# Kernel optimization log

Hardware: AMD Instinct MI355X
Metric: run time of the kernel (lower is better)

## Reference

```python
import jax, jax.numpy as jnp
import numpy as np

B, C, H, W = 4, 48, 512, 512

def gaussian_kernel(kernel_size, channels):
    # matches torch get_gaussian_kernel: sigma from OpenCV rule
    sigma = 0.3 * ((kernel_size - 1) * 0.5 - 1) + 0.8
    grid = np.arange(kernel_size, dtype=np.float32) - kernel_size // 2
    k1 = np.exp(-grid ** 2 / (2 * sigma ** 2))
    k1 /= k1.sum()
    k2 = np.outer(k1, k1)  # [k,k]
    # OIHW depthwise: [C, 1, k, k]
    return jnp.asarray(np.broadcast_to(k2, (channels, 1, kernel_size, kernel_size)))

def depthwise_conv(x, kernel, pad):
    # x: [B,C,H,W], kernel: [C,1,k,k]
    return jax.lax.conv_general_dilated(
        x, kernel,
        window_strides=(1, 1),
        padding=((pad, pad), (pad, pad)),
        dimension_numbers=('NCHW', 'OIHW', 'NCHW'),
        feature_group_count=x.shape[1])

def setup_inputs() -> dict:
    key = jax.random.key(0)
    s = jax.random.normal(key, (B, C, H, W), dtype=jnp.float32)
    one = jnp.ones((), dtype=jnp.float32)
    return {'s': s, 'w1': one, 'w2': one, 'w3': one, 'w4': one}

def reference(s, w1, w2, w3, w4):
    channels = s.shape[1]
    k3 = gaussian_kernel(3, channels)
    k5 = gaussian_kernel(5, channels)
    k7 = gaussian_kernel(7, channels)
    s3 = depthwise_conv(s, k3, 1)
    s5 = depthwise_conv(s, k5, 2)
    s7 = depthwise_conv(s, k7, 3)
    # fused diff + weighted sum: w1*s + w2*(s-s3) + w3*(s3-s5) + w4*(s5-s7)
    return w1 * s + w2 * (s - s3) + w3 * (s3 - s5) + w4 * (s5 - s7)
```

## Files before the change

### kernel.cpp

```cpp
#include <hip/hip_runtime.h>
#include <math.h>

#define TX 64
#define TY 16
#define IN_W 72
#define IN_H 22

struct GaussCoefs {
    float g3[3];
    float g5[5];
    float g7[7];
};

__global__ __launch_bounds__(256) void mgdf_kernel(
    const float* __restrict__ s,
    const float* __restrict__ w1p, const float* __restrict__ w2p,
    const float* __restrict__ w3p, const float* __restrict__ w4p,
    float* __restrict__ out,
    GaussCoefs gc, int Wd, int Hd)
{
    __shared__ float in_tile[IN_H][IN_W];
    __shared__ float h3s[IN_H][TX];
    __shared__ float h5s[IN_H][TX];
    __shared__ float h7s[IN_H][TX];

    const int tid = threadIdx.x;
    const int plane = blockIdx.z;
    const int x0 = blockIdx.x * TX;
    const int y0 = blockIdx.y * TY;
    const float* sp = s + (size_t)plane * Hd * Wd;

    const float w1 = *w1p, w2 = *w2p, w3 = *w3p, w4 = *w4p;
    const float a0 = w1 + w2;
    const float a3 = w3 - w2;
    const float a5 = w4 - w3;
    const float a7 = -w4;

    for (int c = tid; c < (IN_W / 4) * IN_H; c += 256) {
        const int r  = c / (IN_W / 4);
        const int c4 = c % (IN_W / 4);
        const int gy = y0 - 3 + r;
        const int gx = x0 - 4 + c4 * 4;
        float4 v = make_float4(0.f, 0.f, 0.f, 0.f);
        if (gy >= 0 && gy < Hd) {
            const float* rowp = sp + (size_t)gy * Wd;
            if (gx >= 0 && gx + 3 < Wd) {
                v = *(const float4*)(rowp + gx);
            } else {
                float tmp[4];
                #pragma unroll
                for (int j = 0; j < 4; ++j) {
                    const int x = gx + j;
                    tmp[j] = (x >= 0 && x < Wd) ? rowp[x] : 0.f;
                }
                v = make_float4(tmp[0], tmp[1], tmp[2], tmp[3]);
            }
        }
        *(float4*)&in_tile[r][c4 * 4] = v;
    }
    __syncthreads();

    for (int task = tid; task < IN_H * (TX / 4); task += 256) {
        const int r  = task / (TX / 4);
        const int ch = task % (TX / 4);
        const float* row = &in_tile[r][ch * 4];
        const float4 va = *(const float4*)(row);
        const float4 vb = *(const float4*)(row + 4);
        const float4 vc = *(const float4*)(row + 8);
        const float v[12] = {va.x, va.y, va.z, va.w,
                             vb.x, vb.y, vb.z, vb.w,
                             vc.x, vc.y, vc.z, vc.w};
        float o3[4], o5[4], o7[4];
        #pragma unroll
        for (int j = 0; j < 4; ++j) {
            float h7 = 0.f;
            #pragma unroll
            for (int i = 0; i < 7; ++i) h7 = fmaf(gc.g7[i], v[j + 1 + i], h7);
            float h5 = 0.f;
            #pragma unroll
            for (int i = 0; i < 5; ++i) h5 = fmaf(gc.g5[i], v[j + 2 + i], h5);
            float h3 = 0.f;
            #pragma unroll
            for (int i = 0; i < 3; ++i) h3 = fmaf(gc.g3[i], v[j + 3 + i], h3);
            o3[j] = h3; o5[j] = h5; o7[j] = h7;
        }
        *(float4*)&h3s[r][ch * 4] = make_float4(o3[0], o3[1], o3[2], o3[3]);
        *(float4*)&h5s[r][ch * 4] = make_float4(o5[0], o5[1], o5[2], o5[3]);
        *(float4*)&h7s[r][ch * 4] = make_float4(o7[0], o7[1], o7[2], o7[3]);
    }
    __syncthreads();

    const int tx = tid & 15;
    const int ty = tid >> 4;
    const int xb = tx * 4;

    float acc3[4] = {0.f, 0.f, 0.f, 0.f};
    float acc5[4] = {0.f, 0.f, 0.f, 0.f};
    float acc7[4] = {0.f, 0.f, 0.f, 0.f};

    #pragma unroll
    for (int i = 0; i < 7; ++i) {
        const float4 hv = *(const float4*)&h7s[ty + i][xb];
        acc7[0] = fmaf(gc.g7[i], hv.x, acc7[0]);
        acc7[1] = fmaf(gc.g7[i], hv.y, acc7[1]);
        acc7[2] = fmaf(gc.g7[i], hv.z, acc7[2]);
        acc7[3] = fmaf(gc.g7[i], hv.w, acc7[3]);
    }
    #pragma unroll
    for (int i = 0; i < 5; ++i) {
        const float4 hv = *(const float4*)&h5s[ty + 1 + i][xb];
        acc5[0] = fmaf(gc.g5[i], hv.x, acc5[0]);
        acc5[1] = fmaf(gc.g5[i], hv.y, acc5[1]);
        acc5[2] = fmaf(gc.g5[i], hv.z, acc5[2]);
        acc5[3] = fmaf(gc.g5[i], hv.w, acc5[3]);
    }
    #pragma unroll
    for (int i = 0; i < 3; ++i) {
        const float4 hv = *(const float4*)&h3s[ty + 2 + i][xb];
        acc3[0] = fmaf(gc.g3[i], hv.x, acc3[0]);
        acc3[1] = fmaf(gc.g3[i], hv.y, acc3[1]);
        acc3[2] = fmaf(gc.g3[i], hv.z, acc3[2]);
        acc3[3] = fmaf(gc.g3[i], hv.w, acc3[3]);
    }

    const float4 sv = *(const float4*)&in_tile[ty + 3][xb + 4];
    float4 o;
    o.x = a0 * sv.x + a3 * acc3[0] + a5 * acc5[0] + a7 * acc7[0];
    o.y = a0 * sv.y + a3 * acc3[1] + a5 * acc5[1] + a7 * acc7[1];
    o.z = a0 * sv.z + a3 * acc3[2] + a5 * acc5[2] + a7 * acc7[2];
    o.w = a0 * sv.w + a3 * acc3[3] + a5 * acc5[3] + a7 * acc7[3];

    float* outp = out + (size_t)plane * Hd * Wd + (size_t)(y0 + ty) * Wd + x0 + xb;
    *(float4*)outp = o;
}

static void fill_gauss(float* g, int k) {
    const double sigma = 0.3 * ((k - 1) * 0.5 - 1.0) + 0.8;
    double t[7], sum = 0.0;
    for (int i = 0; i < k; ++i) {
        const double x = (double)(i - k / 2);
        t[i] = exp(-x * x / (2.0 * sigma * sigma));
        sum += t[i];
    }
    for (int i = 0; i < k; ++i) g[i] = (float)(t[i] / sum);
}

extern "C" void kernel_launch(void* const* d_in, const int* in_sizes, int n_in,
                              void* d_out, int out_size, void* d_ws, size_t ws_size,
                              hipStream_t stream) {
    const float* s  = (const float*)d_in[0];
    const float* w1 = (const float*)d_in[1];
    const float* w2 = (const float*)d_in[2];
    const float* w3 = (const float*)d_in[3];
    const float* w4 = (const float*)d_in[4];
    float* out = (float*)d_out;

    const int Hd = 512, Wd = 512;
    const int planes = in_sizes[0] / (Hd * Wd);

    GaussCoefs gc;
    fill_gauss(gc.g3, 3);
    fill_gauss(gc.g5, 5);
    fill_gauss(gc.g7, 7);

    dim3 grid(Wd / TX, Hd / TY, planes);
    mgdf_kernel<<<grid, 256, 0, stream>>>(s, w1, w2, w3, w4, out, gc, Wd, Hd);
}
```

Baseline: 372.9 us.

## Register-block vertical pass per thread and drop intermediate shared buffers

Each thread now computes eight output rows. It does the horizontal filter on the fly for each of 14 input rows and scatters the results into register accumulators, so the h3/h5/h7 shared arrays and the second barrier are gone. The block tile grows to 128 rows, which cuts the halo overhead from 22/16 to 134/128. The blend weights are folded into the vertical coefficients. In exchange register pressure rises (32 accumulators plus temporaries), the grid has fewer blocks, and the launch-bounds hint now asks for 4 blocks per CU.

```diff
diff --git a/kernel.cpp b/kernel.cpp
--- a/kernel.cpp
+++ b/kernel.cpp
@@ -1,10 +1,11 @@
 #include <hip/hip_runtime.h>
 #include <math.h>
 
-#define TX 64
-#define TY 16
+#define TX   64
+#define RPT  8
+#define TYB  (16 * RPT)
 #define IN_W 72
-#define IN_H 22
+#define IN_H (TYB + 6)
 
 struct GaussCoefs {
     float g3[3];
@@ -12,7 +13,7 @@
     float g7[7];
 };
 
-__global__ __launch_bounds__(256) void mgdf_kernel(
+__global__ __launch_bounds__(256, 4) void mgdf_kernel(
     const float* __restrict__ s,
     const float* __restrict__ w1p, const float* __restrict__ w2p,
     const float* __restrict__ w3p, const float* __restrict__ w4p,
@@ -20,14 +21,11 @@
     GaussCoefs gc, int Wd, int Hd)
 {
     __shared__ float in_tile[IN_H][IN_W];
-    __shared__ float h3s[IN_H][TX];
-    __shared__ float h5s[IN_H][TX];
-    __shared__ float h7s[IN_H][TX];
 
-    const int tid = threadIdx.x;
+    const int tid   = threadIdx.x;
     const int plane = blockIdx.z;
-    const int x0 = blockIdx.x * TX;
-    const int y0 = blockIdx.y * TY;
+    const int x0    = blockIdx.x * TX;
+    const int y0    = blockIdx.y * TYB;
     const float* sp = s + (size_t)plane * Hd * Wd;
 
     const float w1 = *w1p, w2 = *w2p, w3 = *w3p, w4 = *w4p;
@@ -36,7 +34,15 @@
     const float a5 = w4 - w3;
     const float a7 = -w4;
 
-    for (int c = tid; c < (IN_W / 4) * IN_H; c += 256) {
+    float w7v[7], w5v[5], w3v[3];
+    #pragma unroll
+    for (int i = 0; i < 7; ++i) w7v[i] = a7 * gc.g7[i];
+    #pragma unroll
+    for (int i = 0; i < 5; ++i) w5v[i] = a5 * gc.g5[i];
+    #pragma unroll
+    for (int i = 0; i < 3; ++i) w3v[i] = a3 * gc.g3[i];
+
+    for (int c = tid; c < IN_H * (IN_W / 4); c += 256) {
         const int r  = c / (IN_W / 4);
         const int c4 = c % (IN_W / 4);
         const int gy = y0 - 3 + r;
@@ -60,17 +66,28 @@
     }
     __syncthreads();
 
-    for (int task = tid; task < IN_H * (TX / 4); task += 256) {
-        const int r  = task / (TX / 4);
-        const int ch = task % (TX / 4);
-        const float* row = &in_tile[r][ch * 4];
+    const int tx  = tid & 15;
+    const int tyg = tid >> 4;
+    const int ty0 = tyg * RPT;
+    const int xb  = tx * 4;
+
+    float acc[RPT][4];
+    #pragma unroll
+    for (int r = 0; r < RPT; ++r) {
+        acc[r][0] = 0.f; acc[r][1] = 0.f; acc[r][2] = 0.f; acc[r][3] = 0.f;
+    }
+
+    #pragma unroll
+    for (int ri = 0; ri < RPT + 6; ++ri) {
+        const float* row = &in_tile[ty0 + ri][xb];
         const float4 va = *(const float4*)(row);
         const float4 vb = *(const float4*)(row + 4);
         const float4 vc = *(const float4*)(row + 8);
         const float v[12] = {va.x, va.y, va.z, va.w,
                              vb.x, vb.y, vb.z, vb.w,
                              vc.x, vc.y, vc.z, vc.w};
-        float o3[4], o5[4], o7[4];
+
+        float h3v[4], h5v[4], h7v[4], sv[4];
         #pragma unroll
         for (int j = 0; j < 4; ++j) {
             float h7 = 0.f;
@@ -82,56 +99,36 @@
             float h3 = 0.f;
             #pragma unroll
             for (int i = 0; i < 3; ++i) h3 = fmaf(gc.g3[i], v[j + 3 + i], h3);
-            o3[j] = h3; o5[j] = h5; o7[j] = h7;
+            h7v[j] = h7; h5v[j] = h5; h3v[j] = h3; sv[j] = v[j + 4];
         }
-        *(float4*)&h3s[r][ch * 4] = make_float4(o3[0], o3[1], o3[2], o3[3]);
-        *(float4*)&h5s[r][ch * 4] = make_float4(o5[0], o5[1], o5[2], o5[3]);
-        *(float4*)&h7s[r][ch * 4] = make_float4(o7[0], o7[1], o7[2], o7[3]);
-    }
-    __syncthreads();
 
-    const int tx = tid & 15;
-    const int ty = tid >> 4;
-    const int xb = tx * 4;
-
-    float acc3[4] = {0.f, 0.f, 0.f, 0.f};
-    float acc5[4] = {0.f, 0.f, 0.f, 0.f};
-    float acc7[4] = {0.f, 0.f, 0.f, 0.f};
-
-    #pragma unroll
-    for (int i = 0; i < 7; ++i) {
-        const float4 hv = *(const float4*)&h7s[ty + i][xb];
-        acc7[0] = fmaf(gc.g7[i], hv.x, acc7[0]);
-        acc7[1] = fmaf(gc.g7[i], hv.y, acc7[1]);
-        acc7[2] = fmaf(gc.g7[i], hv.z, acc7[2]);
-        acc7[3] = fmaf(gc.g7[i], hv.w, acc7[3]);
-    }
-    #pragma unroll
-    for (int i = 0; i < 5; ++i) {
-        const float4 hv = *(const float4*)&h5s[ty + 1 + i][xb];
-        acc5[0] = fmaf(gc.g5[i], hv.x, acc5[0]);
-        acc5[1] = fmaf(gc.g5[i], hv.y, acc5[1]);
-        acc5[2] = fmaf(gc.g5[i], hv.z, acc5[2]);
-        acc5[3] = fmaf(gc.g5[i], hv.w, acc5[3]);
-    }
-    #pragma unroll
-    for (int i = 0; i < 3; ++i) {
-        const float4 hv = *(const float4*)&h3s[ty + 2 + i][xb];
-        acc3[0] = fmaf(gc.g3[i], hv.x, acc3[0]);
-        acc3[1] = fmaf(gc.g3[i], hv.y, acc3[1]);
-        acc3[2] = fmaf(gc.g3[i], hv.z, acc3[2]);
-        acc3[3] = fmaf(gc.g3[i], hv.w, acc3[3]);
+        #pragma unroll
+        for (int iv = 0; iv < 7; ++iv) {
+            const int yo = ri - iv;
+            if (yo >= 0 && yo < RPT) {
+                #pragma unroll
+                for (int j = 0; j < 4; ++j) {
+                    float t = fmaf(w7v[iv], h7v[j], acc[yo][j]);
+                    if (iv >= 1 && iv <= 5) t = fmaf(w5v[iv - 1], h5v[j], t);
+                    if (iv >= 2 && iv <= 4) t = fmaf(w3v[iv - 2], h3v[j], t);
+                    if (iv == 3)            t = fmaf(a0, sv[j], t);
+                    acc[yo][j] = t;
+                }
+            }
+        }
     }
 
-    const float4 sv = *(const float4*)&in_tile[ty + 3][xb + 4];
-    float4 o;
-    o.x = a0 * sv.x + a3 * acc3[0] + a5 * acc5[0] + a7 * acc7[0];
-    o.y = a0 * sv.y + a3 * acc3[1] + a5 * acc5[1] + a7 * acc7[1];
-    o.z = a0 * sv.z + a3 * acc3[2] + a5 * acc5[2] + a7 * acc7[2];
-    o.w = a0 * sv.w + a3 * acc3[3] + a5 * acc5[3] + a7 * acc7[3];
-
-    float* outp = out + (size_t)plane * Hd * Wd + (size_t)(y0 + ty) * Wd + x0 + xb;
-    *(float4*)outp = o;
+    float* outp = out + (size_t)plane * Hd * Wd;
+    if (x0 + xb < Wd) {
+        #pragma unroll
+        for (int yo = 0; yo < RPT; ++yo) {
+            const int gy = y0 + ty0 + yo;
+            if (gy < Hd) {
+                *(float4*)(outp + (size_t)gy * Wd + x0 + xb) =
+                    make_float4(acc[yo][0], acc[yo][1], acc[yo][2], acc[yo][3]);
+            }
+        }
+    }
 }
 
 static void fill_gauss(float* g, int k) {
@@ -163,6 +160,6 @@
     fill_gauss(gc.g5, 5);
     fill_gauss(gc.g7, 7);
 
-    dim3 grid(Wd / TX, Hd / TY, planes);
+    dim3 grid((Wd + TX - 1) / TX, (Hd + TYB - 1) / TYB, planes);
     mgdf_kernel<<<grid, 256, 0, stream>>>(s, w1, w2, w3, w4, out, gc, Wd, Hd);
 }
```

New measurement: 835.4 us. 124% more time.
